# Performance work log

Hardware: AMD Instinct MI355X
Metric: run time of the kernel (lower is better)

## Reference

```python
import jax, jax.numpy as jnp
import numpy as np

N_NODES = 100000
N_EDGES = 1000000
D_FEAT = 64


def setup_inputs() -> dict:
    key = jax.random.key(0)
    k1, k2, k3 = jax.random.split(key, 3)
    features = jax.random.normal(k1, (N_NODES, D_FEAT), dtype=jnp.float32)
    src = jax.random.randint(k2, (N_EDGES,), 0, N_NODES, dtype=jnp.int64)
    dst = jax.random.randint(k3, (N_EDGES,), 0, N_NODES, dtype=jnp.int64)
    return {"features": features, "src": src, "dst": dst}


def reference(features, src, dst):
    # DGL update_all(copy_u('h','m'), sum('m','h')):
    # out[v] = sum_{(u,v) in E} features[u]
    msgs = features[src]  # [E, D] gather of source node features
    h = jax.ops.segment_sum(msgs, dst, num_segments=N_NODES)  # [N, D] scatter-add
    return h
```

## Files before the change

### kernel.cpp

```cpp
#include <hip/hip_runtime.h>


#define N_NODES   100000
#define N_EDGES   1000000
#define D_FEAT    64
#define NPB       128
#define NPB_SHIFT 7
#define NB        782
#define EPB       8192
#define CH        2048

typedef unsigned int uint;
typedef unsigned short ushort;

__device__ inline ushort f2bf(float f) {
    uint u = __float_as_uint(f);
    uint lsb = (u >> 16) & 1u;
    u += 0x7fffu + lsb;
    return (ushort)(u >> 16);
}

__global__ __launch_bounds__(512) void conv_hist_kernel(const float* __restrict__ feat,
                                                        ushort* __restrict__ bfeat,
                                                        const int* __restrict__ dst,
                                                        int* __restrict__ cnt_table,
                                                        int n4, int n_edges, int pblocks) {
    __shared__ int cnt[NB];
    int t = threadIdx.x;

    if ((int)blockIdx.x >= pblocks) {
        int i = ((int)blockIdx.x - pblocks) * 512 + t;
        if (i < n4) {
            float4 v = ((const float4*)feat)[i];
            ushort4 o;
            o.x = f2bf(v.x); o.y = f2bf(v.y); o.z = f2bf(v.z); o.w = f2bf(v.w);
            ((ushort4*)bfeat)[i] = o;
        }
        return;
    }

    for (int i = t; i < NB; i += 512) cnt[i] = 0;
    __syncthreads();
    int base = blockIdx.x * EPB + t * 4;
#pragma unroll
    for (int step = 0; step < 4; ++step) {
        int idx = base + step * 2048;
        if (idx < n_edges) {
            int4 d = *reinterpret_cast<const int4*>(dst + idx);
            atomicAdd(&cnt[d.x >> NPB_SHIFT], 1);
            atomicAdd(&cnt[d.y >> NPB_SHIFT], 1);
            atomicAdd(&cnt[d.z >> NPB_SHIFT], 1);
            atomicAdd(&cnt[d.w >> NPB_SHIFT], 1);
        }
    }
    __syncthreads();
    for (int b = t; b < NB; b += 512) cnt_table[blockIdx.x * NB + b] = cnt[b];
}

__global__ __launch_bounds__(1024) void scan_kernel(int* __restrict__ cnt_table,
                                                    int* __restrict__ bases,
                                                    int n_edges, int pblocks) {
    __shared__ int lds[1024];
    int t = threadIdx.x;
    int total = 0;
    if (t < NB) {
        int run = 0;
#pragma unroll 4
        for (int pb = 0; pb < pblocks; ++pb) {
            int idx = pb * NB + t;
            int c = cnt_table[idx];
            cnt_table[idx] = run;
            run += c;
        }
        total = run;
    }
    lds[t] = total;
    __syncthreads();
    for (int off = 1; off < 1024; off <<= 1) {
        int u = (t >= off) ? lds[t - off] : 0;
        __syncthreads();
        lds[t] += u;
        __syncthreads();
    }
    if (t < NB) bases[t] = lds[t] - total;
    if (t == 0) bases[NB] = n_edges;
}

__global__ __launch_bounds__(512) void partition_kernel(const int* __restrict__ src,
                                                        const int* __restrict__ dst,
                                                        const int* __restrict__ bases,
                                                        const int* __restrict__ cnt_table,
                                                        int* __restrict__ pairs, int n) {
    __shared__ int cur[NB];
    int t = threadIdx.x;
    for (int b = t; b < NB; b += 512)
        cur[b] = bases[b] + cnt_table[blockIdx.x * NB + b];
    __syncthreads();

    int base = blockIdx.x * EPB + t * 4;
#pragma unroll
    for (int step = 0; step < 4; ++step) {
        int idx = base + step * 2048;
        if (idx < n) {
            int4 s = *reinterpret_cast<const int4*>(src + idx);
            int4 d = *reinterpret_cast<const int4*>(dst + idx);
            int b, p;
            b = d.x >> NPB_SHIFT; p = atomicAdd(&cur[b], 1); pairs[p] = (s.x << NPB_SHIFT) | (d.x & (NPB - 1));
            b = d.y >> NPB_SHIFT; p = atomicAdd(&cur[b], 1); pairs[p] = (s.y << NPB_SHIFT) | (d.y & (NPB - 1));
            b = d.z >> NPB_SHIFT; p = atomicAdd(&cur[b], 1); pairs[p] = (s.z << NPB_SHIFT) | (d.z & (NPB - 1));
            b = d.w >> NPB_SHIFT; p = atomicAdd(&cur[b], 1); pairs[p] = (s.w << NPB_SHIFT) | (d.w & (NPB - 1));
        }
    }
}

__device__ inline float4 bf4_to_f4(uint2 v) {
    float4 r;
    r.x = __uint_as_float(v.x << 16);
    r.y = __uint_as_float(v.x & 0xffff0000u);
    r.z = __uint_as_float(v.y << 16);
    r.w = __uint_as_float(v.y & 0xffff0000u);
    return r;
}

__global__ __launch_bounds__(256) void gather16_kernel(const ushort* __restrict__ bfeat,
                                                       const int* __restrict__ bases,
                                                       const int* __restrict__ pairs,
                                                       float* __restrict__ out,
                                                       int n_nodes) {
    __shared__ int pbuf[CH];
    __shared__ int sorted[CH];
    __shared__ int deg[32];
    __shared__ int sc[32];
    __shared__ int start[33];
    __shared__ int cur[32];

    int bb = blockIdx.x >> 2;
    int q  = blockIdx.x & 3;
    int t = threadIdx.x;
    int grp = t >> 4;
    int l16 = t & 15;
    int lo = bases[bb], hi = bases[bb + 1];
    int node0 = bb * NPB + q * 32;

    bool first = true;
    for (int c = lo; c < hi || first; c += CH) {
        int n = hi - c;
        if (n > CH) n = CH;
        if (n < 0) n = 0;

        if (t < 32) deg[t] = 0;
        __syncthreads();
        for (int i = t; i < n; i += 256) {
            int p = pairs[c + i];
            pbuf[i] = p;
            int r = p & (NPB - 1);
            if ((r >> 5) == q) atomicAdd(&deg[r & 31], 1);
        }
        __syncthreads();
        if (t < 32) sc[t] = deg[t];
        __syncthreads();
        for (int off = 1; off < 32; off <<= 1) {
            int u = (t < 32 && t >= off) ? sc[t - off] : 0;
            __syncthreads();
            if (t < 32) sc[t] += u;
            __syncthreads();
        }
        if (t < 32) { start[t + 1] = sc[t]; cur[t] = sc[t] - deg[t]; }
        if (t == 0) start[0] = 0;
        __syncthreads();
        for (int i = t; i < n; i += 256) {
            int p = pbuf[i];
            int r = p & (NPB - 1);
            if ((r >> 5) == q) {
                int pos = atomicAdd(&cur[r & 31], 1);
                sorted[pos] = p >> NPB_SHIFT;
            }
        }
        __syncthreads();

        for (int r = grp; r < 32; r += 16) {
            int s0 = start[r], e0 = start[r + 1];
            float4 a0 = {0.f, 0.f, 0.f, 0.f}, a1 = a0, a2 = a0, a3 = a0;
            int i = s0;
            for (; i + 4 <= e0; i += 4) {
                int n0 = sorted[i], n1 = sorted[i + 1];
                int n2 = sorted[i + 2], n3 = sorted[i + 3];
                uint2 w0 = *reinterpret_cast<const uint2*>(bfeat + (size_t)n0 * D_FEAT + l16 * 4);
                uint2 w1 = *reinterpret_cast<const uint2*>(bfeat + (size_t)n1 * D_FEAT + l16 * 4);
                uint2 w2 = *reinterpret_cast<const uint2*>(bfeat + (size_t)n2 * D_FEAT + l16 * 4);
                uint2 w3 = *reinterpret_cast<const uint2*>(bfeat + (size_t)n3 * D_FEAT + l16 * 4);
                float4 v0 = bf4_to_f4(w0), v1 = bf4_to_f4(w1);
                float4 v2 = bf4_to_f4(w2), v3 = bf4_to_f4(w3);
                a0.x += v0.x; a0.y += v0.y; a0.z += v0.z; a0.w += v0.w;
                a1.x += v1.x; a1.y += v1.y; a1.z += v1.z; a1.w += v1.w;
                a2.x += v2.x; a2.y += v2.y; a2.z += v2.z; a2.w += v2.w;
                a3.x += v3.x; a3.y += v3.y; a3.z += v3.z; a3.w += v3.w;
            }
            for (; i < e0; ++i) {
                uint2 w = *reinterpret_cast<const uint2*>(bfeat + (size_t)sorted[i] * D_FEAT + l16 * 4);
                float4 v = bf4_to_f4(w);
                a0.x += v.x; a0.y += v.y; a0.z += v.z; a0.w += v.w;
            }
            float4 acc;
            acc.x = (a0.x + a1.x) + (a2.x + a3.x);
            acc.y = (a0.y + a1.y) + (a2.y + a3.y);
            acc.z = (a0.z + a1.z) + (a2.z + a3.z);
            acc.w = (a0.w + a1.w) + (a2.w + a3.w);

            int node = node0 + r;
            if (node < n_nodes) {
                float* o = out + (size_t)node * D_FEAT + l16 * 4;
                if (first) {
                    *reinterpret_cast<float4*>(o) = acc;
                } else {
                    atomicAdd(o + 0, acc.x); atomicAdd(o + 1, acc.y);
                    atomicAdd(o + 2, acc.z); atomicAdd(o + 3, acc.w);
                }
            }
        }
        first = false;
        __syncthreads();
    }
}

__global__ __launch_bounds__(256) void gather32_kernel(const float* __restrict__ feat,
                                                       const int* __restrict__ bases,
                                                       const int* __restrict__ pairs,
                                                       float* __restrict__ out,
                                                       int n_nodes) {
    __shared__ int pbuf[CH];
    __shared__ int sorted[CH];
    __shared__ int deg[32];
    __shared__ int sc[32];
    __shared__ int start[33];
    __shared__ int cur[32];

    int bb = blockIdx.x >> 2;
    int q  = blockIdx.x & 3;
    int t = threadIdx.x;
    int grp = t >> 4, l16 = t & 15;
    int lo = bases[bb], hi = bases[bb + 1];
    int node0 = bb * NPB + q * 32;

    bool first = true;
    for (int c = lo; c < hi || first; c += CH) {
        int n = hi - c;
        if (n > CH) n = CH;
        if (n < 0) n = 0;

        if (t < 32) deg[t] = 0;
        __syncthreads();
        for (int i = t; i < n; i += 256) {
            int p = pairs[c + i];
            pbuf[i] = p;
            int r = p & (NPB - 1);
            if ((r >> 5) == q) atomicAdd(&deg[r & 31], 1);
        }
        __syncthreads();
        if (t < 32) sc[t] = deg[t];
        __syncthreads();
        for (int off = 1; off < 32; off <<= 1) {
            int u = (t < 32 && t >= off) ? sc[t - off] : 0;
            __syncthreads();
            if (t < 32) sc[t] += u;
            __syncthreads();
        }
        if (t < 32) { start[t + 1] = sc[t]; cur[t] = sc[t] - deg[t]; }
        if (t == 0) start[0] = 0;
        __syncthreads();
        for (int i = t; i < n; i += 256) {
            int p = pbuf[i];
            int r = p & (NPB - 1);
            if ((r >> 5) == q) {
                int pos = atomicAdd(&cur[r & 31], 1);
                sorted[pos] = p >> NPB_SHIFT;
            }
        }
        __syncthreads();

        for (int r = grp; r < 32; r += 16) {
            int s0 = start[r], e0 = start[r + 1];
            float4 a0 = {0.f, 0.f, 0.f, 0.f};
            for (int i = s0; i < e0; ++i) {
                const float4 v = *reinterpret_cast<const float4*>(feat + (size_t)sorted[i] * D_FEAT + l16 * 4);
                a0.x += v.x; a0.y += v.y; a0.z += v.z; a0.w += v.w;
            }
            int node = node0 + r;
            if (node < n_nodes) {
                float* o = out + (size_t)node * D_FEAT + l16 * 4;
                if (first) *reinterpret_cast<float4*>(o) = a0;
                else {
                    atomicAdd(o + 0, a0.x); atomicAdd(o + 1, a0.y);
                    atomicAdd(o + 2, a0.z); atomicAdd(o + 3, a0.w);
                }
            }
        }
        first = false;
        __syncthreads();
    }
}

extern "C" void kernel_launch(void* const* d_in, const int* in_sizes, int n_in,
                              void* d_out, int out_size, void* d_ws, size_t ws_size,
                              hipStream_t stream) {
    const float* feat = (const float*)d_in[0];
    const int*   src  = (const int*)d_in[1];
    const int*   dst  = (const int*)d_in[2];
    float*       out  = (float*)d_out;

    const int n_edges = in_sizes[1];
    const int pblocks = (n_edges + EPB - 1) / EPB;
    const int n4 = N_NODES * D_FEAT / 4;
    const int cblocks = (n4 + 511) / 512;

    int* cnt_table = (int*)d_ws;
    int* bases     = cnt_table + (size_t)pblocks * NB;
    int* pairs     = bases + NB + 1;
    size_t int_cnt = (size_t)pblocks * NB + (NB + 1) + (size_t)n_edges;
    size_t bf_off  = (int_cnt * 4 + 7) & ~(size_t)7;
    ushort* bfeat  = (ushort*)((char*)d_ws + bf_off);
    size_t need = bf_off + (size_t)N_NODES * D_FEAT * 2;

    if (ws_size >= need) {
        conv_hist_kernel<<<pblocks + cblocks, 512, 0, stream>>>(feat, bfeat, dst, cnt_table,
                                                                n4, n_edges, pblocks);
        scan_kernel<<<1, 1024, 0, stream>>>(cnt_table, bases, n_edges, pblocks);
        partition_kernel<<<pblocks, 512, 0, stream>>>(src, dst, bases, cnt_table, pairs, n_edges);
        gather16_kernel<<<NB * 4, 256, 0, stream>>>(bfeat, bases, pairs, out, N_NODES);
    } else {
        conv_hist_kernel<<<pblocks, 512, 0, stream>>>(feat, nullptr, dst, cnt_table,
                                                      n4, n_edges, pblocks);
        scan_kernel<<<1, 1024, 0, stream>>>(cnt_table, bases, n_edges, pblocks);
        partition_kernel<<<pblocks, 512, 0, stream>>>(src, dst, bases, cnt_table, pairs, n_edges);
        gather32_kernel<<<NB * 4, 256, 0, stream>>>(feat, bases, pairs, out, N_NODES);
    }
}
```

Before: 74.32 us.

## Shrink edges per block and parallelize bucket-offset scan across many blocks

Cuts edges per histogram/partition block from 8192 to 2048, so those kernels launch four times as many blocks (489 instead of 123), and removes the per-thread edge loop. The old single-block serial column scan over the count table is replaced by a multi-block wavefront scan: each 64-lane wavefront scans one bucket's column with shuffles. A small single-block scan over the bucket totals then produces the global bases. The aim is to remove a long serial single-block scan and raise parallelism, at the cost of a larger count table, one extra launch, and scan_a only handling up to 512 rows.

Measured after the change: 73.00 us. Within noise of the previous version (-1.8%).

```diff
diff --git a/kernel.cpp b/kernel.cpp
--- a/kernel.cpp
+++ b/kernel.cpp
@@ -7,7 +7,7 @@
 #define NPB       128
 #define NPB_SHIFT 7
 #define NB        782
-#define EPB       8192
+#define EPB       2048
 #define CH        2048
 
 typedef unsigned int uint;
@@ -41,40 +41,47 @@
 
     for (int i = t; i < NB; i += 512) cnt[i] = 0;
     __syncthreads();
-    int base = blockIdx.x * EPB + t * 4;
-#pragma unroll
-    for (int step = 0; step < 4; ++step) {
-        int idx = base + step * 2048;
-        if (idx < n_edges) {
-            int4 d = *reinterpret_cast<const int4*>(dst + idx);
-            atomicAdd(&cnt[d.x >> NPB_SHIFT], 1);
-            atomicAdd(&cnt[d.y >> NPB_SHIFT], 1);
-            atomicAdd(&cnt[d.z >> NPB_SHIFT], 1);
-            atomicAdd(&cnt[d.w >> NPB_SHIFT], 1);
-        }
+    int idx = blockIdx.x * EPB + t * 4;
+    if (idx < n_edges) {
+        int4 d = *reinterpret_cast<const int4*>(dst + idx);
+        atomicAdd(&cnt[d.x >> NPB_SHIFT], 1);
+        atomicAdd(&cnt[d.y >> NPB_SHIFT], 1);
+        atomicAdd(&cnt[d.z >> NPB_SHIFT], 1);
+        atomicAdd(&cnt[d.w >> NPB_SHIFT], 1);
     }
     __syncthreads();
     for (int b = t; b < NB; b += 512) cnt_table[blockIdx.x * NB + b] = cnt[b];
 }
 
-__global__ __launch_bounds__(1024) void scan_kernel(int* __restrict__ cnt_table,
-                                                    int* __restrict__ bases,
-                                                    int n_edges, int pblocks) {
+__global__ __launch_bounds__(512) void scan_a_kernel(int* __restrict__ cnt_table,
+                                                     int* __restrict__ btot, int pb_rows) {
+    int t = threadIdx.x;
+    int bucket = blockIdx.x * 8 + (t >> 6);
+    int lane = t & 63;
+    if (bucket >= NB) return;
+    int run = 0;
+#pragma unroll
+    for (int c = 0; c < 8; ++c) {
+        int r = c * 64 + lane;
+        int orig = (r < pb_rows) ? cnt_table[r * NB + bucket] : 0;
+        int v = orig;
+#pragma unroll
+        for (int d = 1; d < 64; d <<= 1) {
+            int u = __shfl_up(v, d);
+            if (lane >= d) v += u;
+        }
+        if (r < pb_rows) cnt_table[r * NB + bucket] = v - orig + run;
+        run += __shfl(v, 63);
+    }
+    if (lane == 0) btot[bucket] = run;
+}
+
+__global__ __launch_bounds__(1024) void scan_b_kernel(const int* __restrict__ btot,
+                                                      int* __restrict__ bases, int n_edges) {
     __shared__ int lds[1024];
     int t = threadIdx.x;
-    int total = 0;
-    if (t < NB) {
-        int run = 0;
-#pragma unroll 4
-        for (int pb = 0; pb < pblocks; ++pb) {
-            int idx = pb * NB + t;
-            int c = cnt_table[idx];
-            cnt_table[idx] = run;
-            run += c;
-        }
-        total = run;
-    }
-    lds[t] = total;
+    int v = (t < NB) ? btot[t] : 0;
+    lds[t] = v;
     __syncthreads();
     for (int off = 1; off < 1024; off <<= 1) {
         int u = (t >= off) ? lds[t - off] : 0;
@@ -82,7 +89,7 @@
         lds[t] += u;
         __syncthreads();
     }
-    if (t < NB) bases[t] = lds[t] - total;
+    if (t < NB) bases[t] = lds[t] - v;
     if (t == 0) bases[NB] = n_edges;
 }
 
@@ -97,19 +104,15 @@
         cur[b] = bases[b] + cnt_table[blockIdx.x * NB + b];
     __syncthreads();
 
-    int base = blockIdx.x * EPB + t * 4;
-#pragma unroll
-    for (int step = 0; step < 4; ++step) {
-        int idx = base + step * 2048;
-        if (idx < n) {
-            int4 s = *reinterpret_cast<const int4*>(src + idx);
-            int4 d = *reinterpret_cast<const int4*>(dst + idx);
-            int b, p;
-            b = d.x >> NPB_SHIFT; p = atomicAdd(&cur[b], 1); pairs[p] = (s.x << NPB_SHIFT) | (d.x & (NPB - 1));
-            b = d.y >> NPB_SHIFT; p = atomicAdd(&cur[b], 1); pairs[p] = (s.y << NPB_SHIFT) | (d.y & (NPB - 1));
-            b = d.z >> NPB_SHIFT; p = atomicAdd(&cur[b], 1); pairs[p] = (s.z << NPB_SHIFT) | (d.z & (NPB - 1));
-            b = d.w >> NPB_SHIFT; p = atomicAdd(&cur[b], 1); pairs[p] = (s.w << NPB_SHIFT) | (d.w & (NPB - 1));
-        }
+    int idx = blockIdx.x * EPB + t * 4;
+    if (idx < n) {
+        int4 s = *reinterpret_cast<const int4*>(src + idx);
+        int4 d = *reinterpret_cast<const int4*>(dst + idx);
+        int b, p;
+        b = d.x >> NPB_SHIFT; p = atomicAdd(&cur[b], 1); pairs[p] = (s.x << NPB_SHIFT) | (d.x & (NPB - 1));
+        b = d.y >> NPB_SHIFT; p = atomicAdd(&cur[b], 1); pairs[p] = (s.y << NPB_SHIFT) | (d.y & (NPB - 1));
+        b = d.z >> NPB_SHIFT; p = atomicAdd(&cur[b], 1); pairs[p] = (s.z << NPB_SHIFT) | (d.z & (NPB - 1));
+        b = d.w >> NPB_SHIFT; p = atomicAdd(&cur[b], 1); pairs[p] = (s.w << NPB_SHIFT) | (d.w & (NPB - 1));
     }
 }
 
@@ -312,11 +315,13 @@
     const int pblocks = (n_edges + EPB - 1) / EPB;
     const int n4 = N_NODES * D_FEAT / 4;
     const int cblocks = (n4 + 511) / 512;
+    const int sablocks = (NB + 7) / 8;
 
     int* cnt_table = (int*)d_ws;
-    int* bases     = cnt_table + (size_t)pblocks * NB;
+    int* btot      = cnt_table + (size_t)pblocks * NB;
+    int* bases     = btot + NB;
     int* pairs     = bases + NB + 1;
-    size_t int_cnt = (size_t)pblocks * NB + (NB + 1) + (size_t)n_edges;
+    size_t int_cnt = (size_t)pblocks * NB + NB + (NB + 1) + (size_t)n_edges;
     size_t bf_off  = (int_cnt * 4 + 7) & ~(size_t)7;
     ushort* bfeat  = (ushort*)((char*)d_ws + bf_off);
     size_t need = bf_off + (size_t)N_NODES * D_FEAT * 2;
@@ -324,13 +329,15 @@
     if (ws_size >= need) {
         conv_hist_kernel<<<pblocks + cblocks, 512, 0, stream>>>(feat, bfeat, dst, cnt_table,
                                                                 n4, n_edges, pblocks);
-        scan_kernel<<<1, 1024, 0, stream>>>(cnt_table, bases, n_edges, pblocks);
+        scan_a_kernel<<<sablocks, 512, 0, stream>>>(cnt_table, btot, pblocks);
+        scan_b_kernel<<<1, 1024, 0, stream>>>(btot, bases, n_edges);
         partition_kernel<<<pblocks, 512, 0, stream>>>(src, dst, bases, cnt_table, pairs, n_edges);
         gather16_kernel<<<NB * 4, 256, 0, stream>>>(bfeat, bases, pairs, out, N_NODES);
     } else {
         conv_hist_kernel<<<pblocks, 512, 0, stream>>>(feat, nullptr, dst, cnt_table,
                                                       n4, n_edges, pblocks);
-        scan_kernel<<<1, 1024, 0, stream>>>(cnt_table, bases, n_edges, pblocks);
+        scan_a_kernel<<<sablocks, 512, 0, stream>>>(cnt_table, btot, pblocks);
+        scan_b_kernel<<<1, 1024, 0, stream>>>(btot, bases, n_edges);
         partition_kernel<<<pblocks, 512, 0, stream>>>(src, dst, bases, cnt_table, pairs, n_edges);
         gather32_kernel<<<NB * 4, 256, 0, stream>>>(feat, bases, pairs, out, N_NODES);
     }
```
